# Performance work log

Measured on AMD Instinct MI355X. Metric: run time of the kernel, lower is better.

The kernel has to match this reference:

```python
import jax, jax.numpy as jnp
import numpy as np

B, T, D, H, W = 2, 16, 64, 64, 64
E, EXP = 4, 2
TWO_D = 2 * D
HID = EXP * TWO_D


def layernorm(x, g, b, eps=1e-5):
    m = x.mean(-1, keepdims=True)
    v = ((x - m) ** 2).mean(-1, keepdims=True)
    return (x - m) / jnp.sqrt(v + eps) * g + b


def pscan(A, X):
    # h_t = A_t * h_{t-1} + X_t, scanned over axis=1 (time); complex-valued.
    def comb(c1, c2):
        a1, x1 = c1
        a2, x2 = c2
        return a1 * a2, a2 * x1 + x2
    return jax.lax.associative_scan(comb, (A, X), axis=1)[1]


def setup_inputs() -> dict:
    key = jax.random.key(0)
    ks = jax.random.split(key, 24)
    def s(i, shape, scale=0.05):
        return jax.random.normal(ks[i], shape, jnp.float32) * scale
    return {
        "x_re": jax.random.normal(ks[0], (B, T, D, H, W), jnp.float32),
        "x_im": jax.random.normal(ks[1], (B, T, D, H, W), jnp.float32),
        "dt": jax.random.uniform(ks[2], (T,), jnp.float32, 0.5, 1.5),
        "ln_s_g": jnp.ones((TWO_D,), jnp.float32),
        "ln_s_b": jnp.zeros((TWO_D,), jnp.float32),
        "conv_w": s(3, (TWO_D, TWO_D, 3, 3)),
        "conv_b": jnp.zeros((TWO_D,), jnp.float32),
        "ln_t_g": jnp.ones((TWO_D,), jnp.float32),
        "ln_t_b": jnp.zeros((TWO_D,), jnp.float32),
        "enc_re": s(4, (D, D)), "enc_im": s(5, (D, D)),
        "dec_re": s(6, (D, D)), "dec_im": s(7, (D, D)),
        "alpha": s(8, (D,), 0.5), "omega": s(9, (D,), 1.0),
        "wg": s(10, (TWO_D, D)), "bg": jnp.zeros((D,), jnp.float32),
        "p_re": s(11, (D, D)), "p_im": s(12, (D, D)),
        "w_drift": s(13, (TWO_D, D)), "b_drift": jnp.zeros((D,), jnp.float32),
        "w_router": s(14, (TWO_D, E)),
        "w1": s(15, (E, TWO_D, HID)), "w2": s(16, (E, HID, TWO_D)),
        "noise_scale": jnp.float32(0.01),
    }


def reference(x_re, x_im, dt, ln_s_g, ln_s_b, conv_w, conv_b, ln_t_g, ln_t_b,
              enc_re, enc_im, dec_re, dec_im, alpha, omega, wg, bg,
              p_re, p_im, w_drift, b_drift, w_router, w1, w2, noise_scale):
    x = x_re + 1j * x_im  # [B,T,D,H,W] complex64
    N = B * T
    xf = x.reshape(N, D, H, W)
    xr = jnp.concatenate([xf.real, xf.imag], axis=1)  # [N,2D,H,W]
    # spatial LayerNorm over channels
    xn = layernorm(xr.transpose(0, 2, 3, 1), ln_s_g, ln_s_b).transpose(0, 3, 1, 2)
    # Clifford spatial conv (standard 3x3 same-conv on stacked re/im channels)
    xs = jax.lax.conv_general_dilated(xn, conv_w, (1, 1), 'SAME',
                                      dimension_numbers=('NCHW', 'OIHW', 'NCHW'))
    xs = xs + conv_b[None, :, None, None]
    x_sc = xs[:, :D] + 1j * xs[:, D:]            # [N,D,H,W]
    x5 = x_sc.reshape(B, T, D, H, W)              # complex
    # basis encode: complex channel mixing
    enc = enc_re + 1j * enc_im
    u_t = jnp.einsum('bthwd,de->bthwe', x5.transpose(0, 1, 3, 4, 2), enc)  # [B,T,H,W,D]

    # ---- global flux tracker (pscan #1) ----
    x_mean = x5.mean(axis=(-2, -1))               # [B,T,D] complex
    feat = jnp.concatenate([x_mean.real, x_mean.imag], axis=-1)  # [B,T,2D]
    gate = jax.nn.sigmoid(feat @ wg + bg)         # [B,T,D]
    flux_A = gate.astype(jnp.complex64)
    flux_X = (1.0 - gate) * x_mean
    flux_state = pscan(flux_A, flux_X)            # [B,T,D]
    flux_out = flux_state @ (p_re + 1j * p_im)    # [B,T,D]
    drift_in = jnp.concatenate([flux_out.real, flux_out.imag], axis=-1)
    drift = drift_in @ w_drift + b_drift          # [B,T,D] (dead code in source; kept for fidelity)
    drift_c = drift[..., : D // 2] + 1j * drift[..., D // 2:]
    del drift_c

    # ---- temporal propagation (pscan #2) ----
    dt_e = dt.reshape(1, T, 1, 1, 1)              # broadcast (B,T,H,W,1)
    lam = -jax.nn.softplus(alpha) + 1j * omega    # [D]
    decay = jnp.exp(lam * dt_e)                   # [1,T,1,1,D]
    forcing = (decay - 1.0) / lam                 # ZOH forcing operator
    u_scaled = u_t * forcing                      # [B,T,H,W,D]
    decay_full = jnp.broadcast_to(decay, (B, T, H, W, D))
    A_time = decay_full.transpose(0, 2, 3, 1, 4).reshape(B * H * W, T, D)
    X_time = u_scaled.transpose(0, 2, 3, 1, 4).reshape(B * H * W, T, D)
    Y = pscan(A_time, X_time)
    u_out = Y.reshape(B, H, W, T, D).transpose(0, 3, 1, 2, 4)  # [B,T,H,W,D]
    # deterministic surrogate for the SDE stochastic term (state-proportional)
    u_out = u_out + noise_scale * jnp.sqrt(dt_e) * u_out
    dec = dec_re + 1j * dec_im
    x_out = jnp.einsum('bthwd,de->bthwe', u_out, dec)  # decode
    x_out = x_out.transpose(0, 1, 4, 2, 3).reshape(N, D, H, W)
    xo_r = jnp.concatenate([x_out.real, x_out.imag], axis=1)
    xo_n = layernorm(xo_r.transpose(0, 2, 3, 1), ln_t_g, ln_t_b)  # [N,H,W,2D]

    # ---- MoE FFN over pixels (soft mixture of experts) ----
    gates = jax.nn.softmax(xo_n @ w_router, axis=-1)  # [N,H,W,E]
    acc = jnp.zeros_like(xo_n)
    for e in range(E):
        h = jax.nn.gelu(xo_n @ w1[e])
        acc = acc + gates[..., e:e + 1] * (h @ w2[e])
    delta = acc[..., :D] + 1j * acc[..., D:]          # [N,H,W,D]
    delta = delta.transpose(0, 3, 1, 2).reshape(B, T, D, H, W)
    return x + delta
```

## Files before the change

kernel.cpp:

```cpp
#include <hip/hip_runtime.h>
#include <hip/hip_bf16.h>

#define BB 2
#define TT 16
#define DD 64
#define HH 64
#define WW 64
#define NPIX 131072


typedef unsigned short u16;
typedef unsigned int u32;
typedef __attribute__((ext_vector_type(8))) short bf16x8;
typedef __attribute__((ext_vector_type(4))) float f32x4;

union U16x8 { uint4 u4; uint2 u2[2]; u16 h[8]; bf16x8 v; };

__device__ __forceinline__ float us2f(u16 u) {
  union { u32 i; float f; } c; c.i = ((u32)u) << 16; return c.f;
}
__device__ __forceinline__ u16 f2us(float f) {
  u32 x = __float_as_uint(f);
  u32 r = x + 0x7fffu + ((x >> 16) & 1u);
  return (u16)(r >> 16);
}
__device__ __forceinline__ u32 cvtpk(float a, float b) {
  u32 pk;
  asm("v_cvt_pk_bf16_f32 %0, %1, %2" : "=v"(pk) : "v"(a), "v"(b));
  return pk;
}

__global__ __launch_bounds__(256) void k0_prep(
    const float* __restrict__ conv_w,
    const float* __restrict__ enc_re, const float* __restrict__ enc_im,
    const float* __restrict__ dec_re, const float* __restrict__ dec_im,
    const float* __restrict__ w1, const float* __restrict__ w2,
    const float* __restrict__ dt, const float* __restrict__ alpha,
    const float* __restrict__ omega, const float* __restrict__ ns_p,
    u16* __restrict__ mencs, u16* __restrict__ mdecs,
    u16* __restrict__ wcs, u16* __restrict__ w1s, u16* __restrict__ w2s,
    float4* __restrict__ scn, float* __restrict__ sct) {
  int idx = blockIdx.x * 256 + threadIdx.x;
  if (idx < 65536) {
    int m = idx >> 15;
    int z = idx & 32767;
    int s = z >> 14;
    int q = z & 16383;
    int j = q & 7, lane = (q >> 3) & 63, ks = (q >> 9) & 3, nt = (q >> 11) & 7;
    int k = ks * 32 + (lane >> 4) * 8 + j;
    int n = nt * 16 + (lane & 15);
    const float* mre = m ? dec_re : enc_re;
    const float* mim = m ? dec_im : enc_im;
    float v;
    if (k < 64) v = (n < 64) ?  mre[k * 64 + n]        : mim[k * 64 + n - 64];
    else        v = (n < 64) ? -mim[(k - 64) * 64 + n] : mre[(k - 64) * 64 + n - 64];
    u16 hi = f2us(v);
    u16 val = s ? f2us(v - us2f(hi)) : hi;
    u16* dst = m ? mdecs : mencs;
    dst[((nt * 8 + s * 4 + ks) * 64 + lane) * 8 + j] = val;
  } else if (idx < 212992) {
    int z = idx - 65536;
    int j = z & 7, lane = (z >> 3) & 63, ks = (z >> 9) & 3, nt = (z >> 11) & 7, tap = z >> 14;
    int ic = ks * 32 + (lane >> 4) * 8 + j;
    int oc = nt * 16 + (lane & 15);
    wcs[z] = f2us(conv_w[(oc * 128 + ic) * 9 + tap]);
  } else if (idx < 344064) {
    int z = idx - 212992;
    int j = z & 7, lane = (z >> 3) & 63, ks = (z >> 9) & 3, nt = (z >> 11) & 15, e = z >> 15;
    int k = ks * 32 + (lane >> 4) * 8 + j;
    int nn = nt * 16 + (lane & 15);
    w1s[z] = f2us(w1[e * 32768 + k * 256 + nn]);
  } else if (idx < 475136) {
    int z = idx - 344064;
    int j = z & 7, lane = (z >> 3) & 63, ks = (z >> 9) & 7, nt = (z >> 12) & 7, e = z >> 15;
    int k = ks * 32 + (lane >> 4) * 8 + j;
    int nn = nt * 16 + (lane & 15);
    w2s[z] = f2us(w2[e * 32768 + k * 128 + nn]);
  } else if (idx < 476160) {
    int z = idx - 475136;
    int t = z >> 6, d = z & 63;
    float a = alpha[d];
    float sp = (a > 20.f) ? a : log1pf(expf(a));
    float lr = -sp, li = omega[d];
    float inv_l2 = 1.0f / (lr * lr + li * li);
    float dtv = dt[t];
    float er = expf(lr * dtv);
    float ang = li * dtv;
    float dr = er * cosf(ang), di = er * sinf(ang);
    float fr = ((dr - 1.f) * lr + di * li) * inv_l2;
    float fi = (di * lr - (dr - 1.f) * li) * inv_l2;
    scn[z] = make_float4(dr, di, fr, fi);
  } else if (idx < 476176) {
    int t = idx - 476160;
    sct[t] = 1.0f + ns_p[0] * sqrtf(dt[t]);
  }
}

__global__ __launch_bounds__(256) void k1_spatial_ln(
    const float* __restrict__ x_re, const float* __restrict__ x_im,
    const float* __restrict__ g, const float* __restrict__ b,
    u16* __restrict__ xn) {
  __shared__ float tile[64 * 129];
  __shared__ float meanA[64], rstdA[64];
  int n = blockIdx.x >> 6, h = blockIdx.x & 63;
  int tid = threadIdx.x;
  for (int k = 0; k < 32; ++k) {
    int flat = tid + k * 256;
    int c = flat >> 6, w = flat & 63;
    float v = (c < 64) ? x_re[n * 262144 + c * 4096 + h * 64 + w]
                       : x_im[n * 262144 + (c - 64) * 4096 + h * 64 + w];
    tile[w * 129 + c] = v;
  }
  __syncthreads();
  int p = tid >> 2, q = tid & 3;
  float s = 0.f, ss = 0.f;
  for (int c = q * 32; c < q * 32 + 32; ++c) {
    float v = tile[p * 129 + c];
    s += v; ss += v * v;
  }
  s += __shfl_xor(s, 1); ss += __shfl_xor(ss, 1);
  s += __shfl_xor(s, 2); ss += __shfl_xor(ss, 2);
  if (q == 0) {
    float m = s * (1.0f / 128.0f);
    float var = ss * (1.0f / 128.0f) - m * m;
    meanA[p] = m; rstdA[p] = rsqrtf(var + 1e-5f);
  }
  __syncthreads();
  int rowbase = (n * 4096 + h * 64) * 128;
  for (int k = 0; k < 32; ++k) {
    int flat = tid + k * 256;
    int pp = flat >> 7, c = flat & 127;
    float v = (tile[pp * 129 + c] - meanA[pp]) * rstdA[pp] * g[c] + b[c];
    xn[rowbase + flat] = f2us(v);
  }
}

__global__ __launch_bounds__(256) void k2_mfma(
    const u16* __restrict__ xn, const u16* __restrict__ wcs,
    const float* __restrict__ conv_b, const u16* __restrict__ ms,
    u16* __restrict__ xs) {
  __shared__ __align__(16) u16 Xs[3 * 66 * 132];
  int tid = threadIdx.x;
  int wave = tid >> 6, lane = tid & 63;
  int quad = lane >> 4, am = lane & 15;
  int n = blockIdx.x >> 6, h = blockIdx.x & 63;

  for (int dh = 0; dh < 3; ++dh) {
    int hs = h + dh - 1;
    bool valid = (hs >= 0) && (hs < 64);
    const u16* src = xn + (n * 4096 + hs * 64) * 128;
    for (int c = 0; c < 4; ++c) {
      int f8 = tid + c * 256;
      int px = f8 >> 4, ch = (f8 & 15) * 8;
      uint2 lo = make_uint2(0, 0), hi = make_uint2(0, 0);
      if (valid) {
        const uint2* s2 = (const uint2*)(src + px * 128 + ch);
        lo = s2[0]; hi = s2[1];
      }
      u16* dst = Xs + (dh * 66 + px + 1) * 132 + ch;
      *(uint2*)dst = lo;
      *(uint2*)(dst + 4) = hi;
    }
  }
  for (int z = tid; z < 792; z += 256) {
    int dh = z / 264, r = z % 264;
    int px = (r < 132) ? 0 : 65;
    Xs[(dh * 66 + px) * 132 + (r % 132)] = 0;
  }
  __syncthreads();

  f32x4 acc[8];
#pragma unroll
  for (int nt = 0; nt < 8; ++nt) {
    float bv = conv_b[nt * 16 + am];
    acc[nt] = (f32x4){bv, bv, bv, bv};
  }
  int mt = wave;
  for (int tap = 0; tap < 9; ++tap) {
    int dh = tap / 3, dw = tap % 3;
    const u16* arow = Xs + (dh * 66 + mt * 16 + am + dw) * 132 + quad * 8;
    bf16x8 a[4];
#pragma unroll
    for (int ks = 0; ks < 4; ++ks) {
      U16x8 t;
      t.u2[0] = *(const uint2*)(arow + ks * 32);
      t.u2[1] = *(const uint2*)(arow + ks * 32 + 4);
      a[ks] = t.v;
    }
    const uint4* wp = (const uint4*)wcs + tap * 2048 + lane;
    uint4 wb[4];
#pragma unroll
    for (int ks = 0; ks < 4; ++ks) wb[ks] = wp[ks * 64];
    for (int nt = 0; nt < 8; ++nt) {
      uint4 wn[4];
      if (nt < 7) {
#pragma unroll
        for (int ks = 0; ks < 4; ++ks) wn[ks] = wp[((nt + 1) * 4 + ks) * 64];
      }
#pragma unroll
      for (int ks = 0; ks < 4; ++ks) {
        U16x8 bf; bf.u4 = wb[ks];
        acc[nt] = __builtin_amdgcn_mfma_f32_16x16x32_bf16(a[ks], bf.v, acc[nt], 0, 0, 0);
      }
      if (nt < 7) {
#pragma unroll
        for (int ks = 0; ks < 4; ++ks) wb[ks] = wn[ks];
      }
    }
  }

  __syncthreads();
  u16* Cs = Xs;
#pragma unroll
  for (int nt = 0; nt < 8; ++nt)
#pragma unroll
    for (int rp = 0; rp < 2; ++rp) {
      u32 pk = cvtpk(acc[nt][2 * rp], acc[nt][2 * rp + 1]);
      Cs[(wave * 16 + quad * 4 + 2 * rp) * 136 + nt * 16 + am]     = (u16)pk;
      Cs[(wave * 16 + quad * 4 + 2 * rp + 1) * 136 + nt * 16 + am] = (u16)(pk >> 16);
    }
  __syncthreads();

  bf16x8 a2[4];
  {
    const u16* crow = Cs + (wave * 16 + am) * 136;
#pragma unroll
    for (int ks = 0; ks < 4; ++ks) {
      U16x8 t; t.u4 = *(const uint4*)(crow + ks * 32 + quad * 8);
      a2[ks] = t.v;
    }
  }
  const uint4* mp = (const uint4*)ms + lane;
  int rowg = n * 4096 + h * 64 + wave * 16;
  for (int p = 0; p < 4; ++p) {
    f32x4 ca = (f32x4){0.f, 0.f, 0.f, 0.f};
    f32x4 cb = (f32x4){0.f, 0.f, 0.f, 0.f};
#pragma unroll
    for (int kk = 0; kk < 8; ++kk) {
      U16x8 b0; b0.u4 = mp[((2 * p) * 8 + kk) * 64];
      U16x8 b1; b1.u4 = mp[((2 * p + 1) * 8 + kk) * 64];
      ca = __builtin_amdgcn_mfma_f32_16x16x32_bf16(a2[kk & 3], b0.v, ca, 0, 0, 0);
      cb = __builtin_amdgcn_mfma_f32_16x16x32_bf16(a2[kk & 3], b1.v, cb, 0, 0, 0);
    }
#pragma unroll
    for (int r = 0; r < 4; ++r) {
      u32 pk = cvtpk(ca[r], cb[r]);
      xs[(rowg + quad * 4 + r) * 128 + (2 * p) * 16 + am]     = (u16)pk;
      xs[(rowg + quad * 4 + r) * 128 + (2 * p + 1) * 16 + am] = (u16)(pk >> 16);
    }
  }
}

__global__ __launch_bounds__(256) void k_scan(
    u16* __restrict__ u, const float4* __restrict__ scn,
    const float* __restrict__ sct) {
  int flat = blockIdx.x * 256 + threadIdx.x;
  int d = flat & 63;
  int hw = (flat >> 6) & 4095;
  int b = flat >> 18;
  float yr = 0.f, yi = 0.f;
  const int stride = 4096 * 128;
  int base0 = b * 16 * stride + hw * 128 + d;
  for (int t = 0; t < 16; ++t) {
    float4 c = scn[t * 64 + d];
    int idx = base0 + t * stride;
    float ur = us2f(u[idx]), ui = us2f(u[idx + 64]);
    float usr = ur * c.z - ui * c.w;
    float usi = ur * c.w + ui * c.z;
    float nyr = c.x * yr - c.y * yi + usr;
    float nyi = c.x * yi + c.y * yr + usi;
    yr = nyr; yi = nyi;
    float sc = sct[t];
    u32 pk = cvtpk(yr * sc, yi * sc);
    u[idx]      = (u16)pk;
    u[idx + 64] = (u16)(pk >> 16);
  }
}

__global__ __launch_bounds__(256) void k4_mfma(
    const u16* __restrict__ U, const u16* __restrict__ ms,
    const float* __restrict__ g, const float* __restrict__ bb,
    u16* __restrict__ xo) {
  int tid = threadIdx.x;
  int wave = tid >> 6, lane = tid & 63;
  int quad = lane >> 4, am = lane & 15;
  int rowbase = blockIdx.x * 128 + wave * 32;

  bf16x8 ax[2][4];
#pragma unroll
  for (int mt = 0; mt < 2; ++mt) {
    const uint4* ar = (const uint4*)(U + (rowbase + mt * 16 + am) * 128 + quad * 8);
#pragma unroll
    for (int ks = 0; ks < 4; ++ks) { U16x8 t; t.u4 = ar[ks * 4]; ax[mt][ks] = t.v; }
  }
  float gv[8], bv[8];
#pragma unroll
  for (int nt = 0; nt < 8; ++nt) { gv[nt] = g[nt * 16 + am]; bv[nt] = bb[nt * 16 + am]; }

  const uint4* mp = (const uint4*)ms + lane;
  f32x4 acc[2][8];
#pragma unroll
  for (int mt = 0; mt < 2; ++mt)
#pragma unroll
    for (int nt = 0; nt < 8; ++nt) acc[mt][nt] = (f32x4){0.f, 0.f, 0.f, 0.f};

  uint4 wb[8];
#pragma unroll
  for (int kk = 0; kk < 8; ++kk) wb[kk] = mp[kk * 64];
  for (int nt = 0; nt < 8; ++nt) {
    uint4 wn[8];
    if (nt < 7) {
#pragma unroll
      for (int kk = 0; kk < 8; ++kk) wn[kk] = mp[((nt + 1) * 8 + kk) * 64];
    }
#pragma unroll
    for (int kk = 0; kk < 8; ++kk) {
      U16x8 bf; bf.u4 = wb[kk];
      acc[0][nt] = __builtin_amdgcn_mfma_f32_16x16x32_bf16(ax[0][kk & 3], bf.v, acc[0][nt], 0, 0, 0);
      acc[1][nt] = __builtin_amdgcn_mfma_f32_16x16x32_bf16(ax[1][kk & 3], bf.v, acc[1][nt], 0, 0, 0);
    }
    if (nt < 7) {
#pragma unroll
      for (int kk = 0; kk < 8; ++kk) wb[kk] = wn[kk];
    }
  }

#pragma unroll
  for (int mt = 0; mt < 2; ++mt) {
#pragma unroll
    for (int r = 0; r < 4; ++r) {
      float s = 0.f, ss = 0.f;
#pragma unroll
      for (int nt = 0; nt < 8; ++nt) { float v = acc[mt][nt][r]; s += v; ss += v * v; }
      s += __shfl_xor(s, 1); ss += __shfl_xor(ss, 1);
      s += __shfl_xor(s, 2); ss += __shfl_xor(ss, 2);
      s += __shfl_xor(s, 4); ss += __shfl_xor(ss, 4);
      s += __shfl_xor(s, 8); ss += __shfl_xor(ss, 8);
      float m = s * (1.0f / 128.0f);
      float var = ss * (1.0f / 128.0f) - m * m;
      float rstd = rsqrtf(var + 1e-5f);
      u16* xop = xo + (rowbase + mt * 16 + quad * 4 + r) * 128 + am;
#pragma unroll
      for (int n2 = 0; n2 < 4; ++n2) {
        float v0 = (acc[mt][2 * n2][r] - m) * rstd * gv[2 * n2] + bv[2 * n2];
        float v1 = (acc[mt][2 * n2 + 1][r] - m) * rstd * gv[2 * n2 + 1] + bv[2 * n2 + 1];
        u32 pk = cvtpk(v0, v1);
        xop[(2 * n2) * 16]     = (u16)pk;
        xop[(2 * n2 + 1) * 16] = (u16)(pk >> 16);
      }
    }
  }
}

__global__ __launch_bounds__(256) void k5_mfma(
    const u16* __restrict__ xo, const u16* __restrict__ w1s,
    const u16* __restrict__ w2s, const float* __restrict__ w_router,
    const float* __restrict__ x_re, const float* __restrict__ x_im,
    u16* __restrict__ out) {
  __shared__ __align__(16) u16 Hs[128 * 280];
  __shared__ float gate_s[128 * 4];
  int tid = threadIdx.x;
  int wave = tid >> 6, lane = tid & 63;
  int quad = lane >> 4, am = lane & 15;
  int rowbase = blockIdx.x * 128 + wave * 32;

  for (int pp = 0; pp < 2; ++pp) {
    int pxl = wave * 32 + pp * 16 + am;
    const uint4* xr = (const uint4*)(xo + (blockIdx.x * 128 + pxl) * 128);
    float acc = 0.f;
    for (int c8 = 0; c8 < 16; ++c8) {
      U16x8 t; t.u4 = xr[c8];
#pragma unroll
      for (int j = 0; j < 8; ++j)
        acc += us2f(t.h[j]) * w_router[(c8 * 8 + j) * 4 + quad];
    }
    float mx = fmaxf(acc, __shfl_xor(acc, 16));
    mx = fmaxf(mx, __shfl_xor(mx, 32));
    float ex = __expf(acc - mx);
    float sm = ex + __shfl_xor(ex, 16);
    sm += __shfl_xor(sm, 32);
    gate_s[pxl * 4 + quad] = ex / sm;
  }

  bf16x8 ax[2][4];
#pragma unroll
  for (int mt = 0; mt < 2; ++mt) {
    const uint4* ar = (const uint4*)(xo + (rowbase + mt * 16 + am) * 128 + quad * 8);
#pragma unroll
    for (int ks = 0; ks < 4; ++ks) { U16x8 t; t.u4 = ar[ks * 4]; ax[mt][ks] = t.v; }
  }

  f32x4 c2[2][8];
#pragma unroll
  for (int mt = 0; mt < 2; ++mt)
#pragma unroll
    for (int nt = 0; nt < 8; ++nt) c2[mt][nt] = (f32x4){0.f, 0.f, 0.f, 0.f};

  const float GA2 = 2.3022085f, GB2 = 0.10294348f;

  for (int e = 0; e < 4; ++e) {
    const uint4* w1p = (const uint4*)w1s + e * 4096 + lane;
    uint4 wb[4];
#pragma unroll
    for (int ks = 0; ks < 4; ++ks) wb[ks] = w1p[ks * 64];
    for (int nt = 0; nt < 16; ++nt) {
      uint4 wn[4];
      if (nt < 15) {
#pragma unroll
        for (int ks = 0; ks < 4; ++ks) wn[ks] = w1p[((nt + 1) * 4 + ks) * 64];
      }
      f32x4 c1a = (f32x4){0.f, 0.f, 0.f, 0.f};
      f32x4 c1b = (f32x4){0.f, 0.f, 0.f, 0.f};
#pragma unroll
      for (int ks = 0; ks < 4; ++ks) {
        U16x8 bf; bf.u4 = wb[ks];
        c1a = __builtin_amdgcn_mfma_f32_16x16x32_bf16(ax[0][ks], bf.v, c1a, 0, 0, 0);
        c1b = __builtin_amdgcn_mfma_f32_16x16x32_bf16(ax[1][ks], bf.v, c1b, 0, 0, 0);
      }
#pragma unroll
      for (int r = 0; r < 4; ++r) {
        float v = c1a[r];
        float gv0 = gate_s[(wave * 32 + quad * 4 + r) * 4 + e] * v;
        float rc = __builtin_amdgcn_rcpf(
            1.0f + __builtin_amdgcn_exp2f(v * (GA2 + GB2 * v * v)));
        Hs[(wave * 32 + quad * 4 + r) * 280 + nt * 16 + am] = f2us(gv0 - gv0 * rc);
        v = c1b[r];
        float gv1 = gate_s[(wave * 32 + 16 + quad * 4 + r) * 4 + e] * v;
        rc = __builtin_amdgcn_rcpf(
            1.0f + __builtin_amdgcn_exp2f(v * (GA2 + GB2 * v * v)));
        Hs[(wave * 32 + 16 + quad * 4 + r) * 280 + nt * 16 + am] = f2us(gv1 - gv1 * rc);
      }
      if (nt < 15) {
#pragma unroll
        for (int ks = 0; ks < 4; ++ks) wb[ks] = wn[ks];
      }
    }
    const uint4* w2p = (const uint4*)w2s + e * 4096 + lane;
    uint4 wb2[8];
#pragma unroll
    for (int nt = 0; nt < 8; ++nt) wb2[nt] = w2p[(nt * 8) * 64];
    for (int ks = 0; ks < 8; ++ks) {
      uint4 wn2[8];
      if (ks < 7) {
#pragma unroll
        for (int nt = 0; nt < 8; ++nt) wn2[nt] = w2p[(nt * 8 + ks + 1) * 64];
      }
      U16x8 a2[2];
#pragma unroll
      for (int mt = 0; mt < 2; ++mt)
        a2[mt].u4 = *(const uint4*)(Hs + (wave * 32 + mt * 16 + am) * 280 + ks * 32 + quad * 8);
#pragma unroll
      for (int nt = 0; nt < 8; ++nt) {
        U16x8 bf; bf.u4 = wb2[nt];
        c2[0][nt] = __builtin_amdgcn_mfma_f32_16x16x32_bf16(a2[0].v, bf.v, c2[0][nt], 0, 0, 0);
        c2[1][nt] = __builtin_amdgcn_mfma_f32_16x16x32_bf16(a2[1].v, bf.v, c2[1][nt], 0, 0, 0);
      }
      if (ks < 7) {
#pragma unroll
        for (int nt = 0; nt < 8; ++nt) wb2[nt] = wn2[nt];
      }
    }
  }

  __syncthreads();
  float* Os = (float*)Hs;
#pragma unroll
  for (int nt = 0; nt < 4; ++nt)
#pragma unroll
    for (int mt = 0; mt < 2; ++mt)
#pragma unroll
      for (int r = 0; r < 4; ++r) {
        int pxl = wave * 32 + mt * 16 + quad * 4 + r;
        Os[(nt * 16 + am) * 129 + pxl]      = c2[mt][nt][r];
        Os[(64 + nt * 16 + am) * 129 + pxl] = c2[mt][nt + 4][r];
      }
  __syncthreads();
  int nb  = (blockIdx.x * 128) >> 12;
  int hw0 = (blockIdx.x * 128) & 4095;
#pragma unroll
  for (int k = 0; k < 32; ++k) {
    int flat = tid + k * 256;
    int d = flat >> 7, px = flat & 127;
    int gidx = (nb * 64 + d) * 4096 + hw0 + px;
    float rr = x_re[gidx] + Os[d * 129 + px];
    float ii = x_im[gidx] + Os[(64 + d) * 129 + px];
    ((u32*)out)[gidx] = (u32)f2us(ii) | ((u32)f2us(rr) << 16);
  }
}

extern "C" void kernel_launch(void* const* d_in, const int* in_sizes, int n_in,
                              void* d_out, int out_size, void* d_ws, size_t ws_size,
                              hipStream_t stream) {
  const float* x_re     = (const float*)d_in[0];
  const float* x_im     = (const float*)d_in[1];
  const float* dt       = (const float*)d_in[2];
  const float* ln_s_g   = (const float*)d_in[3];
  const float* ln_s_b   = (const float*)d_in[4];
  const float* conv_w   = (const float*)d_in[5];
  const float* conv_b   = (const float*)d_in[6];
  const float* ln_t_g   = (const float*)d_in[7];
  const float* ln_t_b   = (const float*)d_in[8];
  const float* enc_re   = (const float*)d_in[9];
  const float* enc_im   = (const float*)d_in[10];
  const float* dec_re   = (const float*)d_in[11];
  const float* dec_im   = (const float*)d_in[12];
  const float* alpha    = (const float*)d_in[13];
  const float* omega    = (const float*)d_in[14];
  const float* w_router = (const float*)d_in[21];
  const float* w1       = (const float*)d_in[22];
  const float* w2       = (const float*)d_in[23];
  const float* ns       = (const float*)d_in[24];

  u16*   buf   = (u16*)d_ws;
  u16*   mencs = (u16*)((char*)d_ws + 33554432);
  u16*   mdecs = mencs + 32768;
  u16*   wcs   = mdecs + 32768;
  u16*   w1s   = wcs + 147456;
  u16*   w2s   = w1s + 131072;
  float4* scn  = (float4*)(w2s + 131072);
  float* sct   = (float*)(scn + 1024);
  u16*   outf  = (u16*)d_out;

  k0_prep<<<1861, 256, 0, stream>>>(conv_w, enc_re, enc_im, dec_re, dec_im,
                                    w1, w2, dt, alpha, omega, ns,
                                    mencs, mdecs, wcs, w1s, w2s, scn, sct);
  k1_spatial_ln<<<2048, 256, 0, stream>>>(x_re, x_im, ln_s_g, ln_s_b, buf);
  k2_mfma<<<2048, 256, 0, stream>>>(buf, wcs, conv_b, mencs, outf);
  k_scan<<<2048, 256, 0, stream>>>(outf, scn, sct);
  k4_mfma<<<1024, 256, 0, stream>>>(outf, mdecs, ln_t_g, ln_t_b, buf);
  k5_mfma<<<1024, 256, 0, stream>>>(buf, w1s, w2s, w_router, x_re, x_im, outf);
}
```

Before: 434.8 us.

## Fuse decode+LN kernel into MoE kernel via LDS and vectorize spatial LN I/O

Merges the decode GEMM plus temporal LayerNorm kernel into the MoE FFN kernel. The normalized activations now stay in shared memory instead of making a round trip through global memory, and one launch is removed. The spatial LayerNorm kernel now loads inputs as float4 and stores packed pairs of bf16 values, and the buffers are swapped between stages. The fused kernel adds a block barrier and raises register pressure, which may lower occupancy.

```diff
diff --git a/kernel.cpp b/kernel.cpp
--- a/kernel.cpp
+++ b/kernel.cpp
@@ -104,12 +104,17 @@
   __shared__ float meanA[64], rstdA[64];
   int n = blockIdx.x >> 6, h = blockIdx.x & 63;
   int tid = threadIdx.x;
-  for (int k = 0; k < 32; ++k) {
-    int flat = tid + k * 256;
-    int c = flat >> 6, w = flat & 63;
-    float v = (c < 64) ? x_re[n * 262144 + c * 4096 + h * 64 + w]
-                       : x_im[n * 262144 + (c - 64) * 4096 + h * 64 + w];
-    tile[w * 129 + c] = v;
+#pragma unroll
+  for (int k = 0; k < 8; ++k) {
+    int flat4 = tid + k * 256;
+    int c = flat4 >> 4, w4 = (flat4 & 15) * 4;
+    const float* plane = (c < 64) ? x_re : x_im;
+    int cc = c & 63;
+    float4 v = *(const float4*)(plane + n * 262144 + cc * 4096 + h * 64 + w4);
+    tile[(w4 + 0) * 129 + c] = v.x;
+    tile[(w4 + 1) * 129 + c] = v.y;
+    tile[(w4 + 2) * 129 + c] = v.z;
+    tile[(w4 + 3) * 129 + c] = v.w;
   }
   __syncthreads();
   int p = tid >> 2, q = tid & 3;
@@ -126,12 +131,16 @@
     meanA[p] = m; rstdA[p] = rsqrtf(var + 1e-5f);
   }
   __syncthreads();
-  int rowbase = (n * 4096 + h * 64) * 128;
-  for (int k = 0; k < 32; ++k) {
-    int flat = tid + k * 256;
-    int pp = flat >> 7, c = flat & 127;
-    float v = (tile[pp * 129 + c] - meanA[pp]) * rstdA[pp] * g[c] + b[c];
-    xn[rowbase + flat] = f2us(v);
+  int rb2 = (n * 4096 + h * 64) * 64;
+  u32* xn2 = (u32*)xn;
+#pragma unroll
+  for (int k = 0; k < 16; ++k) {
+    int flat2 = tid + k * 256;
+    int pp = flat2 >> 6, c2 = (flat2 & 63) * 2;
+    float m = meanA[pp], r = rstdA[pp];
+    float v0 = (tile[pp * 129 + c2] - m) * r * g[c2] + b[c2];
+    float v1 = (tile[pp * 129 + c2 + 1] - m) * r * g[c2 + 1] + b[c2 + 1];
+    xn2[rb2 + flat2] = cvtpk(v0, v1);
   }
 }
 
@@ -277,84 +286,11 @@
   }
 }
 
-__global__ __launch_bounds__(256) void k4_mfma(
+__global__ __launch_bounds__(256) void k45_mfma(
     const u16* __restrict__ U, const u16* __restrict__ ms,
     const float* __restrict__ g, const float* __restrict__ bb,
-    u16* __restrict__ xo) {
-  int tid = threadIdx.x;
-  int wave = tid >> 6, lane = tid & 63;
-  int quad = lane >> 4, am = lane & 15;
-  int rowbase = blockIdx.x * 128 + wave * 32;
-
-  bf16x8 ax[2][4];
-#pragma unroll
-  for (int mt = 0; mt < 2; ++mt) {
-    const uint4* ar = (const uint4*)(U + (rowbase + mt * 16 + am) * 128 + quad * 8);
-#pragma unroll
-    for (int ks = 0; ks < 4; ++ks) { U16x8 t; t.u4 = ar[ks * 4]; ax[mt][ks] = t.v; }
-  }
-  float gv[8], bv[8];
-#pragma unroll
-  for (int nt = 0; nt < 8; ++nt) { gv[nt] = g[nt * 16 + am]; bv[nt] = bb[nt * 16 + am]; }
-
-  const uint4* mp = (const uint4*)ms + lane;
-  f32x4 acc[2][8];
-#pragma unroll
-  for (int mt = 0; mt < 2; ++mt)
-#pragma unroll
-    for (int nt = 0; nt < 8; ++nt) acc[mt][nt] = (f32x4){0.f, 0.f, 0.f, 0.f};
-
-  uint4 wb[8];
-#pragma unroll
-  for (int kk = 0; kk < 8; ++kk) wb[kk] = mp[kk * 64];
-  for (int nt = 0; nt < 8; ++nt) {
-    uint4 wn[8];
-    if (nt < 7) {
-#pragma unroll
-      for (int kk = 0; kk < 8; ++kk) wn[kk] = mp[((nt + 1) * 8 + kk) * 64];
-    }
-#pragma unroll
-    for (int kk = 0; kk < 8; ++kk) {
-      U16x8 bf; bf.u4 = wb[kk];
-      acc[0][nt] = __builtin_amdgcn_mfma_f32_16x16x32_bf16(ax[0][kk & 3], bf.v, acc[0][nt], 0, 0, 0);
-      acc[1][nt] = __builtin_amdgcn_mfma_f32_16x16x32_bf16(ax[1][kk & 3], bf.v, acc[1][nt], 0, 0, 0);
-    }
-    if (nt < 7) {
-#pragma unroll
-      for (int kk = 0; kk < 8; ++kk) wb[kk] = wn[kk];
-    }
-  }
-
-#pragma unroll
-  for (int mt = 0; mt < 2; ++mt) {
-#pragma unroll
-    for (int r = 0; r < 4; ++r) {
-      float s = 0.f, ss = 0.f;
-#pragma unroll
-      for (int nt = 0; nt < 8; ++nt) { float v = acc[mt][nt][r]; s += v; ss += v * v; }
-      s += __shfl_xor(s, 1); ss += __shfl_xor(ss, 1);
-      s += __shfl_xor(s, 2); ss += __shfl_xor(ss, 2);
-      s += __shfl_xor(s, 4); ss += __shfl_xor(ss, 4);
-      s += __shfl_xor(s, 8); ss += __shfl_xor(ss, 8);
-      float m = s * (1.0f / 128.0f);
-      float var = ss * (1.0f / 128.0f) - m * m;
-      float rstd = rsqrtf(var + 1e-5f);
-      u16* xop = xo + (rowbase + mt * 16 + quad * 4 + r) * 128 + am;
-#pragma unroll
-      for (int n2 = 0; n2 < 4; ++n2) {
-        float v0 = (acc[mt][2 * n2][r] - m) * rstd * gv[2 * n2] + bv[2 * n2];
-        float v1 = (acc[mt][2 * n2 + 1][r] - m) * rstd * gv[2 * n2 + 1] + bv[2 * n2 + 1];
-        u32 pk = cvtpk(v0, v1);
-        xop[(2 * n2) * 16]     = (u16)pk;
-        xop[(2 * n2 + 1) * 16] = (u16)(pk >> 16);
-      }
-    }
-  }
-}
-
-__global__ __launch_bounds__(256) void k5_mfma(
-    const u16* __restrict__ xo, const u16* __restrict__ w1s,
-    const u16* __restrict__ w2s, const float* __restrict__ w_router,
+    const u16* __restrict__ w1s, const u16* __restrict__ w2s,
+    const float* __restrict__ w_router,
     const float* __restrict__ x_re, const float* __restrict__ x_im,
     u16* __restrict__ out) {
   __shared__ __align__(16) u16 Hs[128 * 280];
@@ -364,9 +300,80 @@
   int quad = lane >> 4, am = lane & 15;
   int rowbase = blockIdx.x * 128 + wave * 32;
 
+  {
+    bf16x8 ax4[2][4];
+#pragma unroll
+    for (int mt = 0; mt < 2; ++mt) {
+      const uint4* ar = (const uint4*)(U + (rowbase + mt * 16 + am) * 128 + quad * 8);
+#pragma unroll
+      for (int ks = 0; ks < 4; ++ks) { U16x8 t; t.u4 = ar[ks * 4]; ax4[mt][ks] = t.v; }
+    }
+    float gv[8], bv[8];
+#pragma unroll
+    for (int nt = 0; nt < 8; ++nt) { gv[nt] = g[nt * 16 + am]; bv[nt] = bb[nt * 16 + am]; }
+
+    const uint4* mp = (const uint4*)ms + lane;
+    f32x4 acc[2][8];
+#pragma unroll
+    for (int mt = 0; mt < 2; ++mt)
+#pragma unroll
+      for (int nt = 0; nt < 8; ++nt) acc[mt][nt] = (f32x4){0.f, 0.f, 0.f, 0.f};
+
+    uint4 wb[8];
+#pragma unroll
+    for (int kk = 0; kk < 8; ++kk) wb[kk] = mp[kk * 64];
+    for (int nt = 0; nt < 8; ++nt) {
+      uint4 wn[8];
+      if (nt < 7) {
+#pragma unroll
+        for (int kk = 0; kk < 8; ++kk) wn[kk] = mp[((nt + 1) * 8 + kk) * 64];
+      }
+#pragma unroll
+      for (int kk = 0; kk < 8; ++kk) {
+        U16x8 bf; bf.u4 = wb[kk];
+        acc[0][nt] = __builtin_amdgcn_mfma_f32_16x16x32_bf16(ax4[0][kk & 3], bf.v, acc[0][nt], 0, 0, 0);
+        acc[1][nt] = __builtin_amdgcn_mfma_f32_16x16x32_bf16(ax4[1][kk & 3], bf.v, acc[1][nt], 0, 0, 0);
+      }
+      if (nt < 7) {
+#pragma unroll
+        for (int kk = 0; kk < 8; ++kk) wb[kk] = wn[kk];
+      }
+    }
+
+    u16* Cs = Hs;
+#pragma unroll
+    for (int mt = 0; mt < 2; ++mt) {
+#pragma unroll
+      for (int r = 0; r < 4; ++r) {
+        float s = 0.f, ss = 0.f;
+#pragma unroll
+        for (int nt = 0; nt < 8; ++nt) { float v = acc[mt][nt][r]; s += v; ss += v * v; }
+        s += __shfl_xor(s, 1); ss += __shfl_xor(ss, 1);
+        s += __shfl_xor(s, 2); ss += __shfl_xor(ss, 2);
+        s += __shfl_xor(s, 4); ss += __shfl_xor(ss, 4);
+        s += __shfl_xor(s, 8); ss += __shfl_xor(ss, 8);
+        float m = s * (1.0f / 128.0f);
+        float var = ss * (1.0f / 128.0f) - m * m;
+        float rstd = rsqrtf(var + 1e-5f);
+        u16* crow = Cs + (wave * 32 + mt * 16 + quad * 4 + r) * 136 + am;
+#pragma unroll
+        for (int n2 = 0; n2 < 4; ++n2) {
+          float v0 = (acc[mt][2 * n2][r] - m) * rstd * gv[2 * n2] + bv[2 * n2];
+          float v1 = (acc[mt][2 * n2 + 1][r] - m) * rstd * gv[2 * n2 + 1] + bv[2 * n2 + 1];
+          u32 pk = cvtpk(v0, v1);
+          crow[(2 * n2) * 16]     = (u16)pk;
+          crow[(2 * n2 + 1) * 16] = (u16)(pk >> 16);
+        }
+      }
+    }
+  }
+  __syncthreads();
+
+  const u16* Cs = Hs;
+
   for (int pp = 0; pp < 2; ++pp) {
     int pxl = wave * 32 + pp * 16 + am;
-    const uint4* xr = (const uint4*)(xo + (blockIdx.x * 128 + pxl) * 128);
+    const uint4* xr = (const uint4*)(Cs + pxl * 136);
     float acc = 0.f;
     for (int c8 = 0; c8 < 16; ++c8) {
       U16x8 t; t.u4 = xr[c8];
@@ -385,10 +392,14 @@
   bf16x8 ax[2][4];
 #pragma unroll
   for (int mt = 0; mt < 2; ++mt) {
-    const uint4* ar = (const uint4*)(xo + (rowbase + mt * 16 + am) * 128 + quad * 8);
-#pragma unroll
-    for (int ks = 0; ks < 4; ++ks) { U16x8 t; t.u4 = ar[ks * 4]; ax[mt][ks] = t.v; }
-  }
+    const u16* car = Cs + (wave * 32 + mt * 16 + am) * 136 + quad * 8;
+#pragma unroll
+    for (int ks = 0; ks < 4; ++ks) {
+      U16x8 t; t.u4 = *(const uint4*)(car + ks * 32);
+      ax[mt][ks] = t.v;
+    }
+  }
+  __syncthreads();
 
   f32x4 c2[2][8];
 #pragma unroll
@@ -524,9 +535,9 @@
   k0_prep<<<1861, 256, 0, stream>>>(conv_w, enc_re, enc_im, dec_re, dec_im,
                                     w1, w2, dt, alpha, omega, ns,
                                     mencs, mdecs, wcs, w1s, w2s, scn, sct);
-  k1_spatial_ln<<<2048, 256, 0, stream>>>(x_re, x_im, ln_s_g, ln_s_b, buf);
-  k2_mfma<<<2048, 256, 0, stream>>>(buf, wcs, conv_b, mencs, outf);
-  k_scan<<<2048, 256, 0, stream>>>(outf, scn, sct);
-  k4_mfma<<<1024, 256, 0, stream>>>(outf, mdecs, ln_t_g, ln_t_b, buf);
-  k5_mfma<<<1024, 256, 0, stream>>>(buf, w1s, w2s, w_router, x_re, x_im, outf);
-}
+  k1_spatial_ln<<<2048, 256, 0, stream>>>(x_re, x_im, ln_s_g, ln_s_b, outf);
+  k2_mfma<<<2048, 256, 0, stream>>>(outf, wcs, conv_b, mencs, buf);
+  k_scan<<<2048, 256, 0, stream>>>(buf, scn, sct);
+  k45_mfma<<<1024, 256, 0, stream>>>(buf, mdecs, ln_t_g, ln_t_b,
+                                     w1s, w2s, w_router, x_re, x_im, outf);
+}
```

New measurement: 464.4 us. +6.8%, slower.
